# Performance work log

Hardware: AMD Instinct MI355X
Metric: run time of the kernel (lower is better)

Reference implementation:

```python
import jax, jax.numpy as jnp
import numpy as np

B, A, D, E = 32, 1024, 384, 4   # batch, atoms, descriptor dim, n_elements
H1, H2 = 256, 192               # n_hidden = [256, 192]


def setup_inputs() -> dict:
    key = jax.random.key(0)
    ks = jax.random.split(key, 8)
    representation = jax.random.normal(ks[0], (B, A, D), dtype=jnp.float32)
    species = jax.random.randint(ks[1], (B, A), 0, E, dtype=jnp.int32)
    s = 0.05
    W1 = jax.random.normal(ks[2], (E, D, H1), dtype=jnp.float32) * s
    b1 = jax.random.normal(ks[3], (E, H1), dtype=jnp.float32) * s
    Wh = jax.random.normal(ks[4], (E, H1, H2), dtype=jnp.float32) * s
    bh = jax.random.normal(ks[5], (E, H2), dtype=jnp.float32) * s
    W2 = jax.random.normal(ks[6], (E, H2), dtype=jnp.float32) * s
    b2 = jax.random.normal(ks[7], (E,), dtype=jnp.float32) * s
    return {"representation": representation, "species": species,
            "W1": W1, "b1": b1, "Wh": Wh, "bh": bh, "W2": W2, "b2": b2}


def reference(representation, species, W1, b1, Wh, bh, W2, b2):
    # Dense compute of ALL element nets for every atom (faithful to torch code).
    # MLP: layer1 output is NOT activated (quirk of the original forward);
    # activation only applies to the intermediate `layers` list entries.
    h = jnp.einsum('bad,edh->baeh', representation, W1) + b1          # [B,A,E,H1]
    h = jax.nn.relu(jnp.einsum('baeh,ehk->baek', h, Wh) + bh)         # [B,A,E,H2]
    element_energies = jnp.einsum('baek,ek->bae', h, W2) + b2         # [B,A,E]
    onehot = jax.nn.one_hot(species, E, dtype=element_energies.dtype) # [B,A,E]
    energies = jnp.sum(onehot * element_energies, axis=(1, 2))        # [B]
    return energies
```

## Files before the change

### kernel.cpp

```cpp
#include <hip/hip_runtime.h>

typedef __attribute__((ext_vector_type(8))) short bf16x8;
typedef __attribute__((ext_vector_type(4))) float f32x4;
typedef unsigned short ushort_t;

#define NB 32
#define NA 1024
#define NATOMS (NB*NA)
#define D  384
#define H1 256
#define H2 192
#define NE 4
#define TA 32
#define NGRID 1027

__device__ __forceinline__ ushort_t f2bf(float f) {
    union { float f; unsigned u; } v; v.f = f;
    unsigned r = v.u + 0x7FFF + ((v.u >> 16) & 1);
    return (ushort_t)(r >> 16);
}

__global__ __launch_bounds__(256) void scatter_kernel(
    const int* __restrict__ species, int* __restrict__ counts, int* __restrict__ bucket)
{
    __shared__ int wcnt[4][4];
    __shared__ int wbase[4][4];
    const int t = threadIdx.x, lane = t & 63, wv = t >> 6;
    const int i = blockIdx.x * 256 + t;
    const int e = species[i];

    unsigned long long m0 = __ballot(e == 0);
    unsigned long long m1 = __ballot(e == 1);
    unsigned long long m2 = __ballot(e == 2);
    unsigned long long m3 = __ballot(e == 3);
    unsigned long long mym = (e == 0) ? m0 : (e == 1) ? m1 : (e == 2) ? m2 : m3;
    const unsigned long long lt = (lane == 63) ? 0x7FFFFFFFFFFFFFFFull
                                               : ((1ull << lane) - 1ull);
    const int rank = __popcll(mym & lt);

    if (lane == 0) {
        wcnt[wv][0] = __popcll(m0); wcnt[wv][1] = __popcll(m1);
        wcnt[wv][2] = __popcll(m2); wcnt[wv][3] = __popcll(m3);
    }
    __syncthreads();
    if (t < NE) {
        int s = t;
        int tot = wcnt[0][s] + wcnt[1][s] + wcnt[2][s] + wcnt[3][s];
        int b = atomicAdd(&counts[s], tot);
        for (int w = 0; w < 4; ++w) { wbase[w][s] = b; b += wcnt[w][s]; }
    }
    __syncthreads();
    bucket[(e << 15) + wbase[wv][e] + rank] = i;
}

__global__ __launch_bounds__(256) void transpose_kernel(
    const float* __restrict__ W1, const float* __restrict__ Wh,
    ushort_t* __restrict__ w1t, ushort_t* __restrict__ wht,
    int* __restrict__ counts)
{
    if (blockIdx.x == 0 && threadIdx.x < NE) counts[threadIdx.x] = 0;
    __shared__ float tile[32][33];
    const int t = threadIdx.x;
    int bid = blockIdx.x;
    const float* src; ushort_t* dst; int R, C, e, rt, ct;
    if (bid < NE * 96) {
        e = bid / 96; int rem = bid % 96; rt = rem / 8; ct = rem % 8;
        src = W1; dst = w1t; R = D; C = H1;
    } else {
        bid -= NE * 96;
        e = bid / 48; int rem = bid % 48; rt = rem / 6; ct = rem % 6;
        src = Wh; dst = wht; R = H1; C = H2;
    }
    const float* S  = src + ((size_t)e * R + rt * 32) * C + ct * 32;
    ushort_t*    Dp = dst + ((size_t)e * C + ct * 32) * R + rt * 32;
    {
        int row = t >> 3, c4 = (t & 7) * 4;
        float4 v = *(const float4*)(S + (size_t)row * C + c4);
        tile[row][c4 + 0] = v.x; tile[row][c4 + 1] = v.y;
        tile[row][c4 + 2] = v.z; tile[row][c4 + 3] = v.w;
    }
    __syncthreads();
    {
        int orow = t >> 3, k4 = (t & 7) * 4;
        ushort4 o;
        o.x = f2bf(tile[k4 + 0][orow]);
        o.y = f2bf(tile[k4 + 1][orow]);
        o.z = f2bf(tile[k4 + 2][orow]);
        o.w = f2bf(tile[k4 + 3][orow]);
        *(ushort4*)(Dp + (size_t)orow * R + k4) = o;
    }
}

__global__ __launch_bounds__(256, 4) void mlp_kernel(
    const float*    __restrict__ rep,
    const int*      __restrict__ counts,
    const int*      __restrict__ bucket,
    const ushort_t* __restrict__ w1t,
    const ushort_t* __restrict__ wht,
    const float*    __restrict__ b1,
    const float*    __restrict__ bh,
    const float*    __restrict__ W2,
    const float*    __restrict__ b2,
    float*          __restrict__ energy)
{
    const int c0 = counts[0], c1 = counts[1], c2 = counts[2], c3 = counts[3];
    const int t0 = (c0 + 31) >> 5, t1 = (c1 + 31) >> 5, t2 = (c2 + 31) >> 5;
    const int t3 = (c3 + 31) >> 5;
    int bid = blockIdx.x;
    int e, tile, n;
    if      (bid < t0)                { e = 0; tile = bid;                n = c0; }
    else if (bid < t0 + t1)           { e = 1; tile = bid - t0;           n = c1; }
    else if (bid < t0 + t1 + t2)      { e = 2; tile = bid - t0 - t1;      n = c2; }
    else if (bid < t0 + t1 + t2 + t3) { e = 3; tile = bid - t0 - t1 - t2; n = c3; }
    else return;
    const int base = tile * TA;

    const int t    = threadIdx.x;
    const int lane = t & 63;
    const int wv   = t >> 6;
    const int g    = lane >> 4;
    const int r    = lane & 15;
    const int r7   = r & 7;

    __shared__ ushort_t smem[TA * D + TA * H1];
    ushort_t* Xt  = smem;
    ushort_t* H1t = smem + TA * D;
    float*    eparts = (float*)smem;

    {
        const int srow = t >> 3, scs = t & 7, sswz = srow & 7;
        int ai = base + srow;
        int gs = bucket[(e << 15) + (ai < n ? ai : base)];
        const float* xp = rep + (size_t)gs * D;
        #pragma unroll
        for (int i = 0; i < 6; ++i) {
            const int cs = scs + 8 * i;
            float4 v0 = *(const float4*)(xp + cs * 8);
            float4 v1 = *(const float4*)(xp + cs * 8 + 4);
            union { bf16x8 v; ushort_t u[8]; } pk;
            pk.u[0] = f2bf(v0.x); pk.u[1] = f2bf(v0.y);
            pk.u[2] = f2bf(v0.z); pk.u[3] = f2bf(v0.w);
            pk.u[4] = f2bf(v1.x); pk.u[5] = f2bf(v1.y);
            pk.u[6] = f2bf(v1.z); pk.u[7] = f2bf(v1.w);
            *(bf16x8*)(Xt + srow * D + ((cs ^ sswz) << 3)) = pk.v;
        }
    }
    __syncthreads();

    const ushort_t* a1p = w1t + ((size_t)e * H1 + wv * 64 + r) * D + g * 8;

    f32x4 acc1[4][2];
    #pragma unroll
    for (int nn = 0; nn < 4; ++nn)
        #pragma unroll
        for (int m = 0; m < 2; ++m)
            acc1[nn][m] = (f32x4){0.f, 0.f, 0.f, 0.f};

    #pragma unroll 4
    for (int ks = 0; ks < 12; ++ks) {
        bf16x8 bx[2];
        #pragma unroll
        for (int m = 0; m < 2; ++m) {
            const int cs = ks * 4 + g;
            bx[m] = *(const bf16x8*)(Xt + (m * 16 + r) * D + ((cs ^ r7) << 3));
        }
        #pragma unroll
        for (int nn = 0; nn < 4; ++nn) {
            bf16x8 aw = *(const bf16x8*)(a1p + (size_t)nn * 16 * D + ks * 32);
            #pragma unroll
            for (int m = 0; m < 2; ++m)
                acc1[nn][m] = __builtin_amdgcn_mfma_f32_16x16x32_bf16(
                    aw, bx[m], acc1[nn][m], 0, 0, 0);
        }
    }

    #pragma unroll
    for (int nn = 0; nn < 4; ++nn) {
        float bv[4];
        #pragma unroll
        for (int q = 0; q < 4; ++q)
            bv[q] = b1[e * H1 + wv * 64 + nn * 16 + g * 4 + q];
        #pragma unroll
        for (int m = 0; m < 2; ++m) {
            unsigned p0 = f2bf(acc1[nn][m][0] + bv[0]);
            unsigned p1 = f2bf(acc1[nn][m][1] + bv[1]);
            unsigned p2 = f2bf(acc1[nn][m][2] + bv[2]);
            unsigned p3 = f2bf(acc1[nn][m][3] + bv[3]);
            uint2 pk; pk.x = p0 | (p1 << 16); pk.y = p2 | (p3 << 16);
            const int col = wv * 64 + nn * 16 + g * 4;
            const int cs  = col >> 3;
            const int phys = (m * 16 + r) * H1 + ((cs ^ r7) << 3) + (col & 7);
            *(uint2*)(H1t + phys) = pk;
        }
    }
    __syncthreads();

    const ushort_t* a2p = wht + ((size_t)e * H2 + wv * 48 + r) * H1 + g * 8;

    f32x4 acc2[3][2];
    #pragma unroll
    for (int nn = 0; nn < 3; ++nn)
        #pragma unroll
        for (int m = 0; m < 2; ++m)
            acc2[nn][m] = (f32x4){0.f, 0.f, 0.f, 0.f};

    #pragma unroll 4
    for (int ks = 0; ks < 8; ++ks) {
        bf16x8 bx[2];
        #pragma unroll
        for (int m = 0; m < 2; ++m) {
            const int cs = ks * 4 + g;
            bx[m] = *(const bf16x8*)(H1t + (m * 16 + r) * H1 + ((cs ^ r7) << 3));
        }
        #pragma unroll
        for (int nn = 0; nn < 3; ++nn) {
            bf16x8 aw = *(const bf16x8*)(a2p + (size_t)nn * 16 * H1 + ks * 32);
            #pragma unroll
            for (int m = 0; m < 2; ++m)
                acc2[nn][m] = __builtin_amdgcn_mfma_f32_16x16x32_bf16(
                    aw, bx[m], acc2[nn][m], 0, 0, 0);
        }
    }

    float s2[2] = {0.f, 0.f};
    #pragma unroll
    for (int nn = 0; nn < 3; ++nn) {
        float bhv[4], w2v[4];
        #pragma unroll
        for (int q = 0; q < 4; ++q) {
            int h2i = e * H2 + wv * 48 + nn * 16 + g * 4 + q;
            bhv[q] = bh[h2i];
            w2v[q] = W2[h2i];
        }
        #pragma unroll
        for (int m = 0; m < 2; ++m)
            #pragma unroll
            for (int q = 0; q < 4; ++q) {
                float z = acc2[nn][m][q] + bhv[q];
                z = fmaxf(z, 0.f);
                s2[m] += z * w2v[q];
            }
    }
    #pragma unroll
    for (int m = 0; m < 2; ++m) {
        float s = s2[m];
        s += __shfl_xor(s, 16, 64);
        s += __shfl_xor(s, 32, 64);
        if (lane < 16) eparts[wv * TA + m * 16 + r] = s;
    }
    __syncthreads();
    if (t < TA) {
        int ai = base + t;
        if (ai < n) {
            int gi = bucket[(e << 15) + ai];
            energy[gi] = eparts[t] + eparts[TA + t] + eparts[2 * TA + t]
                       + eparts[3 * TA + t] + b2[e];
        }
    }
}

__global__ void reduce_kernel(const float* __restrict__ energy, float* __restrict__ out) {
    const int b = blockIdx.x, t = threadIdx.x;
    float s = 0.f;
    for (int i = t; i < NA; i += 256) s += energy[b * NA + i];
    for (int off = 32; off > 0; off >>= 1) s += __shfl_down(s, off, 64);
    __shared__ float ws[4];
    if ((t & 63) == 0) ws[t >> 6] = s;
    __syncthreads();
    if (t == 0) out[b] = ws[0] + ws[1] + ws[2] + ws[3];
}

extern "C" void kernel_launch(void* const* d_in, const int* in_sizes, int n_in,
                              void* d_out, int out_size, void* d_ws, size_t ws_size,
                              hipStream_t stream) {
    const float* rep     = (const float*)d_in[0];
    const int*   species = (const int*)  d_in[1];
    const float* W1      = (const float*)d_in[2];
    const float* b1      = (const float*)d_in[3];
    const float* Wh      = (const float*)d_in[4];
    const float* bh      = (const float*)d_in[5];
    const float* W2      = (const float*)d_in[6];
    const float* b2      = (const float*)d_in[7];
    float* out = (float*)d_out;

    char* ws = (char*)d_ws;
    int*      counts  = (int*)      (ws + 0);
    int*      bucket  = (int*)      (ws + 64);
    float*    energy  = (float*)    (ws + 524352);
    ushort_t* w1t     = (ushort_t*) (ws + 655424);
    ushort_t* wht     = (ushort_t*) (ws + 1441856);

    transpose_kernel<<<NE * 96 + NE * 48, 256, 0, stream>>>(W1, Wh, w1t, wht, counts);
    scatter_kernel<<<NATOMS / 256, 256, 0, stream>>>(species, counts, bucket);
    mlp_kernel<<<NGRID, 256, 0, stream>>>(rep, counts, bucket, w1t, wht,
                                          b1, bh, W2, b2, energy);
    reduce_kernel<<<NB, 256, 0, stream>>>(energy, out);
}
```

Measured before the change: 142.1 us.

## Double atom tile to 64 with 512-thread blocks, prefetch weights, alias LDS

The atom tile per block grows from 32 to 64 and the block from 256 to 512 threads (8 waves). Each wave now owns 32 output columns across 4 atom sub-tiles, so every weight fragment loaded from global memory feeds more MFMAs. Weight fragments are software-prefetched one k-step ahead, and the k-loop start is rotated by block index to spread L2 traffic. The H1 buffer reuses the X shared-memory region behind an extra barrier, which keeps LDS near its old size; in layer 2 only 6 of the 8 waves do work, and there are half as many blocks.

```diff
diff --git a/kernel.cpp b/kernel.cpp
--- a/kernel.cpp
+++ b/kernel.cpp
@@ -11,8 +11,8 @@
 #define H1 256
 #define H2 192
 #define NE 4
-#define TA 32
-#define NGRID 1027
+#define TA 64
+#define NGRID 515
 
 __device__ __forceinline__ ushort_t f2bf(float f) {
     union { float f; unsigned u; } v; v.f = f;
@@ -91,7 +91,7 @@
     }
 }
 
-__global__ __launch_bounds__(256, 4) void mlp_kernel(
+__global__ __launch_bounds__(512, 4) void mlp_kernel(
     const float*    __restrict__ rep,
     const int*      __restrict__ counts,
     const int*      __restrict__ bucket,
@@ -104,8 +104,8 @@
     float*          __restrict__ energy)
 {
     const int c0 = counts[0], c1 = counts[1], c2 = counts[2], c3 = counts[3];
-    const int t0 = (c0 + 31) >> 5, t1 = (c1 + 31) >> 5, t2 = (c2 + 31) >> 5;
-    const int t3 = (c3 + 31) >> 5;
+    const int t0 = (c0 + 63) >> 6, t1 = (c1 + 63) >> 6, t2 = (c2 + 63) >> 6;
+    const int t3 = (c3 + 63) >> 6;
     int bid = blockIdx.x;
     int e, tile, n;
     if      (bid < t0)                { e = 0; tile = bid;                n = c0; }
@@ -122,10 +122,10 @@
     const int r    = lane & 15;
     const int r7   = r & 7;
 
-    __shared__ ushort_t smem[TA * D + TA * H1];
+    __shared__ ushort_t smem[TA * D];
     ushort_t* Xt  = smem;
-    ushort_t* H1t = smem + TA * D;
-    float*    eparts = (float*)smem;
+    ushort_t* H1t = smem;
+    float*    eparts = (float*)(smem + 20480);
 
     {
         const int srow = t >> 3, scs = t & 7, sswz = srow & 7;
@@ -147,47 +147,59 @@
     }
     __syncthreads();
 
-    const ushort_t* a1p = w1t + ((size_t)e * H1 + wv * 64 + r) * D + g * 8;
-
-    f32x4 acc1[4][2];
+    const ushort_t* a1p = w1t + ((size_t)e * H1 + wv * 32 + r) * D + g * 8;
+    const int koff1 = (bid & 3) * 3;
+
+    f32x4 acc1[2][4];
     #pragma unroll
-    for (int nn = 0; nn < 4; ++nn)
-        #pragma unroll
-        for (int m = 0; m < 2; ++m)
+    for (int nn = 0; nn < 2; ++nn)
+        #pragma unroll
+        for (int m = 0; m < 4; ++m)
             acc1[nn][m] = (f32x4){0.f, 0.f, 0.f, 0.f};
 
-    #pragma unroll 4
+    uint4 afc[2], afn[2];
+    {
+        int k0 = koff1 * 32;
+        afc[0] = *(const uint4*)(a1p + k0);
+        afc[1] = *(const uint4*)(a1p + 16 * D + k0);
+    }
     for (int ks = 0; ks < 12; ++ks) {
-        bf16x8 bx[2];
-        #pragma unroll
-        for (int m = 0; m < 2; ++m) {
-            const int cs = ks * 4 + g;
+        int kse = ks + koff1; if (kse >= 12) kse -= 12;
+        if (ks < 11) {
+            int ksn = kse + 1; if (ksn >= 12) ksn -= 12;
+            afn[0] = *(const uint4*)(a1p + ksn * 32);
+            afn[1] = *(const uint4*)(a1p + 16 * D + ksn * 32);
+        }
+        bf16x8 bx[4];
+        #pragma unroll
+        for (int m = 0; m < 4; ++m) {
+            const int cs = kse * 4 + g;
             bx[m] = *(const bf16x8*)(Xt + (m * 16 + r) * D + ((cs ^ r7) << 3));
         }
         #pragma unroll
-        for (int nn = 0; nn < 4; ++nn) {
-            bf16x8 aw = *(const bf16x8*)(a1p + (size_t)nn * 16 * D + ks * 32);
-            #pragma unroll
-            for (int m = 0; m < 2; ++m)
+        for (int nn = 0; nn < 2; ++nn)
+            #pragma unroll
+            for (int m = 0; m < 4; ++m)
                 acc1[nn][m] = __builtin_amdgcn_mfma_f32_16x16x32_bf16(
-                    aw, bx[m], acc1[nn][m], 0, 0, 0);
-        }
-    }
+                    __builtin_bit_cast(bf16x8, afc[nn]), bx[m], acc1[nn][m], 0, 0, 0);
+        afc[0] = afn[0]; afc[1] = afn[1];
+    }
+    __syncthreads();
 
     #pragma unroll
-    for (int nn = 0; nn < 4; ++nn) {
+    for (int nn = 0; nn < 2; ++nn) {
         float bv[4];
         #pragma unroll
         for (int q = 0; q < 4; ++q)
-            bv[q] = b1[e * H1 + wv * 64 + nn * 16 + g * 4 + q];
-        #pragma unroll
-        for (int m = 0; m < 2; ++m) {
+            bv[q] = b1[e * H1 + wv * 32 + nn * 16 + g * 4 + q];
+        #pragma unroll
+        for (int m = 0; m < 4; ++m) {
             unsigned p0 = f2bf(acc1[nn][m][0] + bv[0]);
             unsigned p1 = f2bf(acc1[nn][m][1] + bv[1]);
             unsigned p2 = f2bf(acc1[nn][m][2] + bv[2]);
             unsigned p3 = f2bf(acc1[nn][m][3] + bv[3]);
             uint2 pk; pk.x = p0 | (p1 << 16); pk.y = p2 | (p3 << 16);
-            const int col = wv * 64 + nn * 16 + g * 4;
+            const int col = wv * 32 + nn * 16 + g * 4;
             const int cs  = col >> 3;
             const int phys = (m * 16 + r) * H1 + ((cs ^ r7) << 3) + (col & 7);
             *(uint2*)(H1t + phys) = pk;
@@ -195,66 +207,78 @@
     }
     __syncthreads();
 
-    const ushort_t* a2p = wht + ((size_t)e * H2 + wv * 48 + r) * H1 + g * 8;
-
-    f32x4 acc2[3][2];
+    f32x4 acc2[2][4];
     #pragma unroll
-    for (int nn = 0; nn < 3; ++nn)
-        #pragma unroll
-        for (int m = 0; m < 2; ++m)
+    for (int nn = 0; nn < 2; ++nn)
+        #pragma unroll
+        for (int m = 0; m < 4; ++m)
             acc2[nn][m] = (f32x4){0.f, 0.f, 0.f, 0.f};
 
-    #pragma unroll 4
-    for (int ks = 0; ks < 8; ++ks) {
-        bf16x8 bx[2];
-        #pragma unroll
-        for (int m = 0; m < 2; ++m) {
-            const int cs = ks * 4 + g;
-            bx[m] = *(const bf16x8*)(H1t + (m * 16 + r) * H1 + ((cs ^ r7) << 3));
-        }
-        #pragma unroll
-        for (int nn = 0; nn < 3; ++nn) {
-            bf16x8 aw = *(const bf16x8*)(a2p + (size_t)nn * 16 * H1 + ks * 32);
-            #pragma unroll
-            for (int m = 0; m < 2; ++m)
-                acc2[nn][m] = __builtin_amdgcn_mfma_f32_16x16x32_bf16(
-                    aw, bx[m], acc2[nn][m], 0, 0, 0);
-        }
-    }
-
-    float s2[2] = {0.f, 0.f};
-    #pragma unroll
-    for (int nn = 0; nn < 3; ++nn) {
-        float bhv[4], w2v[4];
-        #pragma unroll
-        for (int q = 0; q < 4; ++q) {
-            int h2i = e * H2 + wv * 48 + nn * 16 + g * 4 + q;
-            bhv[q] = bh[h2i];
-            w2v[q] = W2[h2i];
-        }
-        #pragma unroll
-        for (int m = 0; m < 2; ++m)
-            #pragma unroll
-            for (int q = 0; q < 4; ++q) {
-                float z = acc2[nn][m][q] + bhv[q];
-                z = fmaxf(z, 0.f);
-                s2[m] += z * w2v[q];
+    if (wv < 6) {
+        const ushort_t* a2p = wht + ((size_t)e * H2 + wv * 32 + r) * H1 + g * 8;
+        const int koff2 = (bid & 3) * 2;
+        uint4 af2c[2], af2n[2];
+        {
+            int k0 = koff2 * 32;
+            af2c[0] = *(const uint4*)(a2p + k0);
+            af2c[1] = *(const uint4*)(a2p + 16 * H1 + k0);
+        }
+        for (int ks = 0; ks < 8; ++ks) {
+            int kse = ks + koff2; if (kse >= 8) kse -= 8;
+            if (ks < 7) {
+                int ksn = kse + 1; if (ksn >= 8) ksn -= 8;
+                af2n[0] = *(const uint4*)(a2p + ksn * 32);
+                af2n[1] = *(const uint4*)(a2p + 16 * H1 + ksn * 32);
             }
-    }
-    #pragma unroll
-    for (int m = 0; m < 2; ++m) {
-        float s = s2[m];
-        s += __shfl_xor(s, 16, 64);
-        s += __shfl_xor(s, 32, 64);
-        if (lane < 16) eparts[wv * TA + m * 16 + r] = s;
-    }
-    __syncthreads();
+            bf16x8 bx[4];
+            #pragma unroll
+            for (int m = 0; m < 4; ++m) {
+                const int cs = kse * 4 + g;
+                bx[m] = *(const bf16x8*)(H1t + (m * 16 + r) * H1 + ((cs ^ r7) << 3));
+            }
+            #pragma unroll
+            for (int nn = 0; nn < 2; ++nn)
+                #pragma unroll
+                for (int m = 0; m < 4; ++m)
+                    acc2[nn][m] = __builtin_amdgcn_mfma_f32_16x16x32_bf16(
+                        __builtin_bit_cast(bf16x8, af2c[nn]), bx[m], acc2[nn][m], 0, 0, 0);
+            af2c[0] = af2n[0]; af2c[1] = af2n[1];
+        }
+
+        #pragma unroll
+        for (int m = 0; m < 4; ++m) {
+            float s = 0.f;
+            #pragma unroll
+            for (int nn = 0; nn < 2; ++nn) {
+                float bhv[4], w2v[4];
+                #pragma unroll
+                for (int q = 0; q < 4; ++q) {
+                    int h2i = e * H2 + wv * 32 + nn * 16 + g * 4 + q;
+                    bhv[q] = bh[h2i];
+                    w2v[q] = W2[h2i];
+                }
+                #pragma unroll
+                for (int q = 0; q < 4; ++q) {
+                    float z = acc2[nn][m][q] + bhv[q];
+                    z = fmaxf(z, 0.f);
+                    s += z * w2v[q];
+                }
+            }
+            s += __shfl_xor(s, 16, 64);
+            s += __shfl_xor(s, 32, 64);
+            if (lane < 16) eparts[wv * TA + m * 16 + r] = s;
+        }
+    }
+    __syncthreads();
+
     if (t < TA) {
         int ai = base + t;
         if (ai < n) {
             int gi = bucket[(e << 15) + ai];
-            energy[gi] = eparts[t] + eparts[TA + t] + eparts[2 * TA + t]
-                       + eparts[3 * TA + t] + b2[e];
+            float tot = b2[e];
+            #pragma unroll
+            for (int w = 0; w < 6; ++w) tot += eparts[w * TA + t];
+            energy[gi] = tot;
         }
     }
 }
@@ -292,7 +316,7 @@
 
     transpose_kernel<<<NE * 96 + NE * 48, 256, 0, stream>>>(W1, Wh, w1t, wht, counts);
     scatter_kernel<<<NATOMS / 256, 256, 0, stream>>>(species, counts, bucket);
-    mlp_kernel<<<NGRID, 256, 0, stream>>>(rep, counts, bucket, w1t, wht,
+    mlp_kernel<<<NGRID, 512, 0, stream>>>(rep, counts, bucket, w1t, wht,
                                           b1, bh, W2, b2, energy);
     reduce_kernel<<<NB, 256, 0, stream>>>(energy, out);
 }
```

Result: faster. 127.0 us (-10.6%).
